# Kernel tuning notes

Hardware: AMD Instinct MI355X
Metric: run time of the kernel (lower is better)

Reference implementation:

```python
import jax, jax.numpy as jnp
import numpy as np

FOV_UP = 3.0 * np.pi / 180.0
FOV_DOWN = -25.0 * np.pi / 180.0
BIG = 1e9  # penalty to exclude invalid points from nearest-neighbor search


def rv_to_points(rv):
    """Spherical back-projection of a range image [H,W] -> xyz [H,W,3]."""
    H, W = rv.shape
    fov = FOV_UP - FOV_DOWN
    pitch = (1.0 - (jnp.arange(H, dtype=rv.dtype) + 0.5) / H) * fov + FOV_DOWN  # [H]
    yaw = -((jnp.arange(W, dtype=rv.dtype) + 0.5) / W * 2.0 - 1.0) * jnp.pi     # [W]
    cp = jnp.cos(pitch)[:, None]
    sp = jnp.sin(pitch)[:, None]
    x = rv * cp * jnp.cos(yaw)[None, :]
    y = rv * cp * jnp.sin(yaw)[None, :]
    z = rv * sp
    return jnp.stack([x, y, z], axis=-1)


def masked_chamfer(po, mo, pt, mt):
    """Symmetric chamfer (squared distances) between masked point sets.
    po [N,3], mo [N] in {0,1}; pt [M,3], mt [M] in {0,1}."""
    # squared pairwise distances [N,M] without materializing [N,M,3]
    d = (jnp.sum(po * po, axis=-1)[:, None]
         + jnp.sum(pt * pt, axis=-1)[None, :]
         - 2.0 * po @ pt.T)
    d1 = jnp.min(d + BIG * (1.0 - mt)[None, :], axis=1)  # NN dist for each output pt
    d2 = jnp.min(d + BIG * (1.0 - mo)[:, None], axis=0)  # NN dist for each target pt
    m1 = jnp.sum(d1 * mo) / jnp.maximum(jnp.sum(mo), 1.0)
    m2 = jnp.sum(d2 * mt) / jnp.maximum(jnp.sum(mt), 1.0)
    return m1 + m2


def chamfer_forward(rv, target):
    B, S, H, W = rv.shape

    def one(args):
        rv_bs, tgt_bs = args  # [H,W], [4,H,W]
        po = rv_to_points(rv_bs).reshape(-1, 3)
        mo = (rv_bs > 0.0).astype(rv_bs.dtype).reshape(-1)
        pt = jnp.transpose(tgt_bs[1:4], (1, 2, 0)).reshape(-1, 3)
        mt = (tgt_bs[0] > 0.0).astype(rv_bs.dtype).reshape(-1)
        return masked_chamfer(po, mo, pt, mt)

    # sequential over the B*S pairs: only one [N,N] distance matrix live at a time
    per_pair = jax.lax.map(one, (rv.reshape(B * S, H, W),
                                 target.reshape(B * S, 4, H, W)))
    return per_pair.reshape(B, S).T  # [S, B], matches chamfer_distances_tensor[s, b]


def setup_inputs():
    key = jax.random.key(0)
    k1, k2, k3 = jax.random.split(key, 3)
    B, S, H, W = 2, 4, 64, 128
    rv = jax.random.normal(k1, (B, S, H, W), dtype=jnp.float32)
    target = jax.random.normal(k2, (B, S, 4, H, W), dtype=jnp.float32)
    mos_label = jax.random.randint(k3, (B, S, H, W), 0, 2, dtype=jnp.int32)
    return {"rv": rv, "target": target, "mos_label": mos_label, "n_samples": -1}


def reference(rv, target, mos_label, n_samples):
    # n_samples == -1 -> full (non-subsampled) chamfer distance.
    # mos_label is extracted in the original but never affects the returned values.
    tensor = chamfer_forward(rv, target)          # [S, B]
    per_step = jnp.mean(tensor, axis=1)           # chamfer_distances[s] = batch mean
    return per_step, tensor
```

## Files before the change

kernel.cpp:

```cpp
#include <hip/hip_runtime.h>
#include <math.h>

constexpr int kH = 64, kW = 128, kB = 2, kS = 4;
constexpr int kNP = kH * kW;
constexpr int kPairs = kB * kS;
constexpr int kDirs = kPairs * 2;
constexpr float kPen = 32768.0f;
constexpr float kPi = 3.14159265358979323846f;
constexpr float kFovUp = 3.0f * kPi / 180.0f;
constexpr float kFovDown = -25.0f * kPi / 180.0f;

typedef short short8 __attribute__((ext_vector_type(8)));
typedef unsigned short ushort8 __attribute__((ext_vector_type(8)));
typedef float floatx4 __attribute__((ext_vector_type(4)));

constexpr int NCC = 8;
constexpr int CCH = kNP / NCC;
constexpr int NQB = 16;

constexpr size_t OFF_MIN = 524288;
constexpr size_t OFF_MVAL = 655360;
constexpr size_t OFF_DCNT = 655376;
constexpr size_t OFF_ACNT = 655392;

__device__ __forceinline__ unsigned short f2bf(float v) {
  unsigned u = __float_as_uint(v);
  unsigned r = u + 0x7FFFu + ((u >> 16) & 1u);
  return (unsigned short)(r >> 16);
}
__device__ __forceinline__ float bf2f(unsigned short b) {
  return __uint_as_float(((unsigned)b) << 16);
}


__global__ __launch_bounds__(256) void prep_kernel(
    const float* __restrict__ rv, const float* __restrict__ tgt,
    float4* __restrict__ pts, unsigned* __restrict__ minarr,
    float* __restrict__ mval, unsigned* __restrict__ dcnt,
    unsigned* __restrict__ acnt) {
  int idx = blockIdx.x * 256 + threadIdx.x;
  int p = idx >> 13;
  int k = idx & (kNP - 1);
  int h = k >> 7;
  int w = k & 127;

  float r = rv[idx];
  float pitch = (1.0f - (h + 0.5f) * (1.0f / kH)) * (kFovUp - kFovDown) + kFovDown;
  float yaw = -(((w + 0.5f) * (1.0f / kW)) * 2.0f - 1.0f) * kPi;
  float cp = __cosf(pitch), sp = __sinf(pitch);
  float cy = __cosf(yaw), sy = __sinf(yaw);
  float px = r * cp * cy, py = r * cp * sy, pz = r * sp;
  float mo = (r > 0.0f) ? 1.0f : 0.0f;

  const float* tb = tgt + (size_t)p * 4 * kNP;
  float mt = (tb[k] > 0.0f) ? 1.0f : 0.0f;
  float tx = tb[kNP + k], ty = tb[2 * kNP + k], tz = tb[3 * kNP + k];

  float no = px * px + py * py + pz * pz;
  float nt = tx * tx + ty * ty + tz * tz;
  float co = no + kPen * (1.0f - mo);
  float ct = nt + kPen * (1.0f - mt);

  int d0 = 2 * p, d1 = d0 + 1;
  pts[(size_t)d0 * kNP + k] = make_float4(px, py, pz, co);
  pts[(size_t)d1 * kNP + k] = make_float4(tx, ty, tz, ct);

  minarr[(size_t)d0 * kNP + k] = 0xFFFFFFFFu;
  minarr[(size_t)d1 * kNP + k] = 0xFFFFFFFFu;
  if (idx < kDirs) { dcnt[idx] = 0u; mval[idx] = 0.0f; }
  if (idx == kDirs) *acnt = 0u;
}

__global__ __launch_bounds__(256, 4) void nn_kernel(
    const float4* __restrict__ pts, unsigned* __restrict__ minarr,
    float* __restrict__ mval, unsigned* __restrict__ dcnt,
    unsigned* __restrict__ acnt, float* __restrict__ out) {
  __shared__ __align__(16) unsigned short sc[CCH * 16 + 16];
  __shared__ unsigned s_ticket;
  __shared__ float sw[4], sm[4];

  int bid = blockIdx.x;
  int d = bid >> 7;
  int qb = (bid >> 3) & 15;
  int ch = bid & 7;
  int t = threadIdx.x;

  const float4* cand = pts + (size_t)(d ^ 1) * kNP + ch * CCH;
#pragma unroll
  for (int i = 0; i < 4; ++i) {
    int j = t + i * 256;
    float4 P = cand[j];
    float X = -2.0f * P.x, Y = -2.0f * P.y, Z = -2.0f * P.z;
    float ct = P.w;
    unsigned short Xh = f2bf(X), Yh = f2bf(Y), Zh = f2bf(Z);
    unsigned short Xl = f2bf(X - bf2f(Xh));
    unsigned short Yl = f2bf(Y - bf2f(Yh));
    unsigned short Zl = f2bf(Z - bf2f(Zh));
    unsigned short Ch = f2bf(ct);
    float c1 = ct - bf2f(Ch);
    unsigned short Cl = f2bf(c1);
    unsigned short Cl2 = f2bf(c1 - bf2f(Cl));
    unsigned short* dst = sc + (j >> 4) * 256 + (j & 15) * 8;
    *(ushort8*)dst = (ushort8){Xh, Xl, Xh, Yh, Yl, Yh, Zh, Zl};
    *(ushort8*)(dst + 128) = (ushort8){Zh, Ch, Cl, Cl2, 0, 0, 0, 0};
  }
  if (t < 2) ((float4*)(sc + CCH * 16))[t] = make_float4(0.f, 0.f, 0.f, 0.f);
  __syncthreads();

  int wave = t >> 6, lane = t & 63;
  int n = lane & 15, q = lane >> 4;
  int qbase = d * kNP + qb * 512 + wave * 128;

  const short one_bf = (short)0x3F80;
  short8 bfr[8];
  float mn[8];
#pragma unroll
  for (int i = 0; i < 8; ++i) {
    short8 b = (short8){0, 0, 0, 0, 0, 0, 0, 0};
    if (q < 2) {
      float4 P = pts[qbase + i * 16 + n];
      unsigned short xh = f2bf(P.x), yh = f2bf(P.y), zh = f2bf(P.z);
      unsigned short xl = f2bf(P.x - bf2f(xh));
      unsigned short yl = f2bf(P.y - bf2f(yh));
      unsigned short zl = f2bf(P.z - bf2f(zh));
      if (q == 0)
        b = (short8){(short)xh, (short)xh, (short)xl, (short)yh,
                     (short)yh, (short)yl, (short)zh, (short)zh};
      else
        b = (short8){(short)zl, one_bf, one_bf, one_bf, 0, 0, 0, 0};
    }
    bfr[i] = b;
    mn[i] = 3.0e38f;
  }

  floatx4 zc = {0.0f, 0.0f, 0.0f, 0.0f};
  const unsigned short* aptr = (q < 2) ? (sc + q * 128 + n * 8) : (sc + CCH * 16);
  int astep = (q < 2) ? 256 : 0;

#pragma unroll 2
  for (int ctile = 0; ctile < CCH / 16; ++ctile) {
    short8 a = *(const short8*)aptr;
    aptr += astep;
#pragma unroll
    for (int i = 0; i < 8; ++i) {
      floatx4 dr = __builtin_amdgcn_mfma_f32_16x16x32_bf16(a, bfr[i], zc, 0, 0, 0);
      float u = fminf(fminf(dr[0], dr[1]), dr[2]);
      mn[i] = fminf(fminf(u, dr[3]), mn[i]);
    }
  }

#pragma unroll
  for (int i = 0; i < 8; ++i) {
    float m = mn[i];
    m = fminf(m, __shfl_xor(m, 16));
    m = fminf(m, __shfl_xor(m, 32));
    if (lane < 16) {
      unsigned bb = __float_as_uint(m);
      unsigned e = (bb & 0x80000000u) ? ~bb : (bb | 0x80000000u);
      atomicMin(&minarr[qbase + i * 16 + lane], e);
    }
  }

  __syncthreads();
  if (t == 0)
    s_ticket = __hip_atomic_fetch_add(&dcnt[d], 1u, __ATOMIC_RELAXED,
                                      __HIP_MEMORY_SCOPE_AGENT);
  __syncthreads();
  if (s_ticket != 127u) return;

  float wsum = 0.0f, msum = 0.0f;
#pragma unroll 4
  for (int j = 0; j < 32; ++j) {
    int k = j * 256 + t;
    unsigned u = __hip_atomic_load(&minarr[(size_t)d * kNP + k],
                                   __ATOMIC_RELAXED, __HIP_MEMORY_SCOPE_AGENT);
    unsigned bb = (u & 0x80000000u) ? (u ^ 0x80000000u) : ~u;
    float mnv = __uint_as_float(bb);
    float4 P = pts[(size_t)d * kNP + k];
    if (P.w < 16384.0f) {
      wsum += P.w + mnv;
      msum += 1.0f;
    }
  }
#pragma unroll
  for (int off = 32; off; off >>= 1) {
    wsum += __shfl_down(wsum, off);
    msum += __shfl_down(msum, off);
  }
  if ((t & 63) == 0) { sw[t >> 6] = wsum; sm[t >> 6] = msum; }
  __syncthreads();
  if (t == 0) {
    float ws_ = sw[0] + sw[1] + sw[2] + sw[3];
    float ms_ = sm[0] + sm[1] + sm[2] + sm[3];
    __hip_atomic_store(&mval[d], ws_ / fmaxf(ms_, 1.0f), __ATOMIC_RELAXED,
                       __HIP_MEMORY_SCOPE_AGENT);
    s_ticket = __hip_atomic_fetch_add(acnt, 1u, __ATOMIC_ACQ_REL,
                                      __HIP_MEMORY_SCOPE_AGENT);
  }
  __syncthreads();
  if (s_ticket != (unsigned)(kDirs - 1)) return;
  if (t == 0) {
    float mv[kDirs];
    for (int dd = 0; dd < kDirs; ++dd)
      mv[dd] = __hip_atomic_load(&mval[dd], __ATOMIC_RELAXED,
                                 __HIP_MEMORY_SCOPE_AGENT);
    for (int s = 0; s < kS; ++s) {
      float acc = 0.0f;
      for (int b = 0; b < kB; ++b) {
        int p = b * kS + s;
        float tens = mv[2 * p] + mv[2 * p + 1];
        out[kS + s * kB + b] = tens;
        acc += tens;
      }
      out[s] = acc * (1.0f / kB);
    }
  }
}

extern "C" void kernel_launch(void* const* d_in, const int* in_sizes, int n_in,
                              void* d_out, int out_size, void* d_ws, size_t ws_size,
                              hipStream_t stream) {
  const float* rv = (const float*)d_in[0];
  const float* tgt = (const float*)d_in[1];
  float* ws = (float*)d_ws;
  float4* pts = (float4*)ws;
  unsigned* minarr = (unsigned*)(ws + OFF_MIN);
  float* mval = ws + OFF_MVAL;
  unsigned* dcnt = (unsigned*)(ws + OFF_DCNT);
  unsigned* acnt = (unsigned*)(ws + OFF_ACNT);
  float* out = (float*)d_out;

  hipLaunchKernelGGL(prep_kernel, dim3(kPairs * kNP / 256), dim3(256), 0, stream,
                     rv, tgt, pts, minarr, mval, dcnt, acnt);
  hipLaunchKernelGGL(nn_kernel, dim3(kDirs * NQB * NCC), dim3(256), 0, stream,
                     pts, minarr, mval, dcnt, acnt, out);
}
```

Measured before the change: 116.6 us.

## Compute both chamfer directions from one distance tile with full-distance MFMA

The per-query norm is now folded into the MFMA operands, so each tile holds full squared distances. One pass per pair can then reduce both the row minima (output-to-target) and the column minima (target-to-output). Column minima are reduced with cross-lane shuffles into LDS atomics and then merged into global memory, which halves the grid and the total MFMA work. A constant bias keeps every distance positive so that raw float bit patterns can be used for atomicMin without the sign-flip encoding. The cost is extra shuffles and LDS atomics per tile in the inner loop.

```diff
diff --git a/kernel.cpp b/kernel.cpp
--- a/kernel.cpp
+++ b/kernel.cpp
@@ -6,6 +6,7 @@
 constexpr int kPairs = kB * kS;
 constexpr int kDirs = kPairs * 2;
 constexpr float kPen = 32768.0f;
+constexpr float kBias = 0.25f;
 constexpr float kPi = 3.14159265358979323846f;
 constexpr float kFovUp = 3.0f * kPi / 180.0f;
 constexpr float kFovDown = -25.0f * kPi / 180.0f;
@@ -17,6 +18,7 @@
 constexpr int NCC = 8;
 constexpr int CCH = kNP / NCC;
 constexpr int NQB = 16;
+constexpr int BPP = NQB * NCC;
 
 constexpr size_t OFF_MIN = 524288;
 constexpr size_t OFF_MVAL = 655360;
@@ -58,8 +60,8 @@
 
   float no = px * px + py * py + pz * pz;
   float nt = tx * tx + ty * ty + tz * tz;
-  float co = no + kPen * (1.0f - mo);
-  float ct = nt + kPen * (1.0f - mt);
+  float co = no + kPen * (1.0f - mo) + kBias;
+  float ct = nt + kPen * (1.0f - mt) + kBias;
 
   int d0 = 2 * p, d1 = d0 + 1;
   pts[(size_t)d0 * kNP + k] = make_float4(px, py, pz, co);
@@ -76,16 +78,19 @@
     float* __restrict__ mval, unsigned* __restrict__ dcnt,
     unsigned* __restrict__ acnt, float* __restrict__ out) {
   __shared__ __align__(16) unsigned short sc[CCH * 16 + 16];
+  __shared__ unsigned cminLds[CCH];
   __shared__ unsigned s_ticket;
-  __shared__ float sw[4], sm[4];
+  __shared__ float sred[16];
 
   int bid = blockIdx.x;
-  int d = bid >> 7;
+  int dp = bid >> 7;
+  int d0 = 2 * dp, d1 = d0 + 1;
   int qb = (bid >> 3) & 15;
   int ch = bid & 7;
   int t = threadIdx.x;
 
-  const float4* cand = pts + (size_t)(d ^ 1) * kNP + ch * CCH;
+  const float4* cand = pts + (size_t)d1 * kNP + ch * CCH;
+  const unsigned short one_bfu = 0x3F80;
 #pragma unroll
   for (int i = 0; i < 4; ++i) {
     int j = t + i * 256;
@@ -102,14 +107,17 @@
     unsigned short Cl2 = f2bf(c1 - bf2f(Cl));
     unsigned short* dst = sc + (j >> 4) * 256 + (j & 15) * 8;
     *(ushort8*)dst = (ushort8){Xh, Xl, Xh, Yh, Yl, Yh, Zh, Zl};
-    *(ushort8*)(dst + 128) = (ushort8){Zh, Ch, Cl, Cl2, 0, 0, 0, 0};
-  }
+    *(ushort8*)(dst + 128) =
+        (ushort8){Zh, Ch, Cl, Cl2, one_bfu, one_bfu, one_bfu, 0};
+  }
+#pragma unroll
+  for (int i = 0; i < 4; ++i) cminLds[t + i * 256] = 0xFFFFFFFFu;
   if (t < 2) ((float4*)(sc + CCH * 16))[t] = make_float4(0.f, 0.f, 0.f, 0.f);
   __syncthreads();
 
   int wave = t >> 6, lane = t & 63;
   int n = lane & 15, q = lane >> 4;
-  int qbase = d * kNP + qb * 512 + wave * 128;
+  int qbase = d0 * kNP + qb * 512 + wave * 128;
 
   const short one_bf = (short)0x3F80;
   short8 bfr[8];
@@ -123,11 +131,17 @@
       unsigned short xl = f2bf(P.x - bf2f(xh));
       unsigned short yl = f2bf(P.y - bf2f(yh));
       unsigned short zl = f2bf(P.z - bf2f(zh));
-      if (q == 0)
+      if (q == 0) {
         b = (short8){(short)xh, (short)xh, (short)xl, (short)yh,
                      (short)yh, (short)yl, (short)zh, (short)zh};
-      else
-        b = (short8){(short)zl, one_bf, one_bf, one_bf, 0, 0, 0, 0};
+      } else {
+        unsigned short Wh = f2bf(P.w);
+        float w1 = P.w - bf2f(Wh);
+        unsigned short Wl = f2bf(w1);
+        unsigned short Wl2 = f2bf(w1 - bf2f(Wl));
+        b = (short8){(short)zl, one_bf, one_bf, one_bf,
+                     (short)Wh, (short)Wl, (short)Wl2, 0};
+      }
     }
     bfr[i] = b;
     mn[i] = 3.0e38f;
@@ -136,16 +150,40 @@
   floatx4 zc = {0.0f, 0.0f, 0.0f, 0.0f};
   const unsigned short* aptr = (q < 2) ? (sc + q * 128 + n * 8) : (sc + CCH * 16);
   int astep = (q < 2) ? 256 : 0;
+  int cq4 = (lane >> 4) * 4;
+  bool leader = (n == 0);
 
 #pragma unroll 2
   for (int ctile = 0; ctile < CCH / 16; ++ctile) {
     short8 a = *(const short8*)aptr;
     aptr += astep;
-#pragma unroll
-    for (int i = 0; i < 8; ++i) {
-      floatx4 dr = __builtin_amdgcn_mfma_f32_16x16x32_bf16(a, bfr[i], zc, 0, 0, 0);
-      float u = fminf(fminf(dr[0], dr[1]), dr[2]);
-      mn[i] = fminf(fminf(u, dr[3]), mn[i]);
+    float c0 = 3.0e38f, c1 = 3.0e38f, c2 = 3.0e38f, c3 = 3.0e38f;
+#pragma unroll
+    for (int i = 0; i < 8; i += 2) {
+      floatx4 dA = __builtin_amdgcn_mfma_f32_16x16x32_bf16(a, bfr[i], zc, 0, 0, 0);
+      floatx4 dB = __builtin_amdgcn_mfma_f32_16x16x32_bf16(a, bfr[i + 1], zc, 0, 0, 0);
+      float uA = fminf(fminf(dA[0], dA[1]), dA[2]);
+      mn[i] = fminf(fminf(uA, dA[3]), mn[i]);
+      float uB = fminf(fminf(dB[0], dB[1]), dB[2]);
+      mn[i + 1] = fminf(fminf(uB, dB[3]), mn[i + 1]);
+      c0 = fminf(fminf(dA[0], dB[0]), c0);
+      c1 = fminf(fminf(dA[1], dB[1]), c1);
+      c2 = fminf(fminf(dA[2], dB[2]), c2);
+      c3 = fminf(fminf(dA[3], dB[3]), c3);
+    }
+#pragma unroll
+    for (int s = 1; s <= 8; s <<= 1) {
+      c0 = fminf(c0, __shfl_xor(c0, s));
+      c1 = fminf(c1, __shfl_xor(c1, s));
+      c2 = fminf(c2, __shfl_xor(c2, s));
+      c3 = fminf(c3, __shfl_xor(c3, s));
+    }
+    if (leader) {
+      unsigned* cp = cminLds + ctile * 16 + cq4;
+      atomicMin(cp + 0, __float_as_uint(c0));
+      atomicMin(cp + 1, __float_as_uint(c1));
+      atomicMin(cp + 2, __float_as_uint(c2));
+      atomicMin(cp + 3, __float_as_uint(c3));
     }
   }
 
@@ -154,51 +192,68 @@
     float m = mn[i];
     m = fminf(m, __shfl_xor(m, 16));
     m = fminf(m, __shfl_xor(m, 32));
-    if (lane < 16) {
-      unsigned bb = __float_as_uint(m);
-      unsigned e = (bb & 0x80000000u) ? ~bb : (bb | 0x80000000u);
-      atomicMin(&minarr[qbase + i * 16 + lane], e);
+    if (lane < 16)
+      atomicMin(&minarr[qbase + i * 16 + lane], __float_as_uint(m));
+  }
+
+  __syncthreads();
+  {
+    unsigned* garr = minarr + (size_t)d1 * kNP + ch * CCH;
+#pragma unroll
+    for (int i = 0; i < 4; ++i) {
+      int c = t + i * 256;
+      atomicMin(&garr[c], cminLds[c]);
     }
   }
 
   __syncthreads();
   if (t == 0)
-    s_ticket = __hip_atomic_fetch_add(&dcnt[d], 1u, __ATOMIC_RELAXED,
+    s_ticket = __hip_atomic_fetch_add(&dcnt[dp], 1u, __ATOMIC_RELAXED,
                                       __HIP_MEMORY_SCOPE_AGENT);
   __syncthreads();
-  if (s_ticket != 127u) return;
-
-  float wsum = 0.0f, msum = 0.0f;
-#pragma unroll 4
+  if (s_ticket != (unsigned)(BPP - 1)) return;
+
+  float ws0 = 0.0f, ms0 = 0.0f, ws1 = 0.0f, ms1 = 0.0f;
+#pragma unroll 2
   for (int j = 0; j < 32; ++j) {
     int k = j * 256 + t;
-    unsigned u = __hip_atomic_load(&minarr[(size_t)d * kNP + k],
-                                   __ATOMIC_RELAXED, __HIP_MEMORY_SCOPE_AGENT);
-    unsigned bb = (u & 0x80000000u) ? (u ^ 0x80000000u) : ~u;
-    float mnv = __uint_as_float(bb);
-    float4 P = pts[(size_t)d * kNP + k];
-    if (P.w < 16384.0f) {
-      wsum += P.w + mnv;
-      msum += 1.0f;
+    {
+      unsigned u = __hip_atomic_load(&minarr[(size_t)d0 * kNP + k],
+                                     __ATOMIC_RELAXED, __HIP_MEMORY_SCOPE_AGENT);
+      float4 P = pts[(size_t)d0 * kNP + k];
+      if (P.w < 16384.0f) { ws0 += __uint_as_float(u) - 2.0f * kBias; ms0 += 1.0f; }
+    }
+    {
+      unsigned u = __hip_atomic_load(&minarr[(size_t)d1 * kNP + k],
+                                     __ATOMIC_RELAXED, __HIP_MEMORY_SCOPE_AGENT);
+      float4 P = pts[(size_t)d1 * kNP + k];
+      if (P.w < 16384.0f) { ws1 += __uint_as_float(u) - 2.0f * kBias; ms1 += 1.0f; }
     }
   }
 #pragma unroll
   for (int off = 32; off; off >>= 1) {
-    wsum += __shfl_down(wsum, off);
-    msum += __shfl_down(msum, off);
-  }
-  if ((t & 63) == 0) { sw[t >> 6] = wsum; sm[t >> 6] = msum; }
+    ws0 += __shfl_down(ws0, off); ms0 += __shfl_down(ms0, off);
+    ws1 += __shfl_down(ws1, off); ms1 += __shfl_down(ms1, off);
+  }
+  if ((t & 63) == 0) {
+    int w = t >> 6;
+    sred[w] = ws0; sred[4 + w] = ms0; sred[8 + w] = ws1; sred[12 + w] = ms1;
+  }
   __syncthreads();
   if (t == 0) {
-    float ws_ = sw[0] + sw[1] + sw[2] + sw[3];
-    float ms_ = sm[0] + sm[1] + sm[2] + sm[3];
-    __hip_atomic_store(&mval[d], ws_ / fmaxf(ms_, 1.0f), __ATOMIC_RELAXED,
+    float W0 = sred[0] + sred[1] + sred[2] + sred[3];
+    float M0 = sred[4] + sred[5] + sred[6] + sred[7];
+    float W1 = sred[8] + sred[9] + sred[10] + sred[11];
+    float M1 = sred[12] + sred[13] + sred[14] + sred[15];
+    __hip_atomic_store(&mval[d0], W0 / fmaxf(M0, 1.0f), __ATOMIC_RELAXED,
+                       __HIP_MEMORY_SCOPE_AGENT);
+    __hip_atomic_store(&mval[d1], W1 / fmaxf(M1, 1.0f), __ATOMIC_RELAXED,
                        __HIP_MEMORY_SCOPE_AGENT);
     s_ticket = __hip_atomic_fetch_add(acnt, 1u, __ATOMIC_ACQ_REL,
                                       __HIP_MEMORY_SCOPE_AGENT);
   }
   __syncthreads();
-  if (s_ticket != (unsigned)(kDirs - 1)) return;
+  if (s_ticket != (unsigned)(kPairs - 1)) return;
   if (t == 0) {
     float mv[kDirs];
     for (int dd = 0; dd < kDirs; ++dd)
@@ -232,6 +287,6 @@
 
   hipLaunchKernelGGL(prep_kernel, dim3(kPairs * kNP / 256), dim3(256), 0, stream,
                      rv, tgt, pts, minarr, mval, dcnt, acnt);
-  hipLaunchKernelGGL(nn_kernel, dim3(kDirs * NQB * NCC), dim3(256), 0, stream,
+  hipLaunchKernelGGL(nn_kernel, dim3(kPairs * NQB * NCC), dim3(256), 0, stream,
                      pts, minarr, mval, dcnt, acnt, out);
 }
```

New measurement: 142.8 us. 1.22x slower.

## Switch distance tiles to 32x32x16 MFMA to remove wasted K lanes

Applied to the files above, without the earlier changes.

Replaces the 16x16x32 bf16 MFMA, whose upper K half was zero padding, with the 32x32x16 variant that packs the 13 split-precision terms into K=16. Query tiling and grid are reorganised to 1024 queries per block, with 32-wide query tiles per wave. The next candidate fragment is prefetched from LDS. This aims to cut wasted matrix-core work per distance, at the cost of more accumulator registers per MFMA and fewer blocks.

```diff
diff --git a/kernel.cpp b/kernel.cpp
--- a/kernel.cpp
+++ b/kernel.cpp
@@ -12,11 +12,13 @@
 
 typedef short short8 __attribute__((ext_vector_type(8)));
 typedef unsigned short ushort8 __attribute__((ext_vector_type(8)));
-typedef float floatx4 __attribute__((ext_vector_type(4)));
+typedef float floatx16 __attribute__((ext_vector_type(16)));
 
 constexpr int NCC = 8;
 constexpr int CCH = kNP / NCC;
-constexpr int NQB = 16;
+constexpr int NQB = 8;
+constexpr int BPD = NQB * NCC;
+constexpr int QT = 8;
 
 constexpr size_t OFF_MIN = 524288;
 constexpr size_t OFF_MVAL = 655360;
@@ -75,13 +77,13 @@
     const float4* __restrict__ pts, unsigned* __restrict__ minarr,
     float* __restrict__ mval, unsigned* __restrict__ dcnt,
     unsigned* __restrict__ acnt, float* __restrict__ out) {
-  __shared__ __align__(16) unsigned short sc[CCH * 16 + 16];
+  __shared__ __align__(16) unsigned short sc[CCH * 16 + 512];
   __shared__ unsigned s_ticket;
   __shared__ float sw[4], sm[4];
 
   int bid = blockIdx.x;
-  int d = bid >> 7;
-  int qb = (bid >> 3) & 15;
+  int d = bid >> 6;
+  int qb = (bid >> 3) & 7;
   int ch = bid & 7;
   int t = threadIdx.x;
 
@@ -100,64 +102,67 @@
     float c1 = ct - bf2f(Ch);
     unsigned short Cl = f2bf(c1);
     unsigned short Cl2 = f2bf(c1 - bf2f(Cl));
-    unsigned short* dst = sc + (j >> 4) * 256 + (j & 15) * 8;
+    unsigned short* dst = sc + (j >> 5) * 512 + (j & 31) * 8;
     *(ushort8*)dst = (ushort8){Xh, Xl, Xh, Yh, Yl, Yh, Zh, Zl};
-    *(ushort8*)(dst + 128) = (ushort8){Zh, Ch, Cl, Cl2, 0, 0, 0, 0};
-  }
-  if (t < 2) ((float4*)(sc + CCH * 16))[t] = make_float4(0.f, 0.f, 0.f, 0.f);
+    *(ushort8*)(dst + 256) = (ushort8){Zh, Ch, Cl, Cl2, 0, 0, 0, 0};
+  }
   __syncthreads();
 
   int wave = t >> 6, lane = t & 63;
-  int n = lane & 15, q = lane >> 4;
-  int qbase = d * kNP + qb * 512 + wave * 128;
+  int col = lane & 31, half = lane >> 5;
+  int qbase = d * kNP + qb * 1024 + wave * 256;
 
   const short one_bf = (short)0x3F80;
-  short8 bfr[8];
-  float mn[8];
-#pragma unroll
-  for (int i = 0; i < 8; ++i) {
-    short8 b = (short8){0, 0, 0, 0, 0, 0, 0, 0};
-    if (q < 2) {
-      float4 P = pts[qbase + i * 16 + n];
-      unsigned short xh = f2bf(P.x), yh = f2bf(P.y), zh = f2bf(P.z);
-      unsigned short xl = f2bf(P.x - bf2f(xh));
-      unsigned short yl = f2bf(P.y - bf2f(yh));
-      unsigned short zl = f2bf(P.z - bf2f(zh));
-      if (q == 0)
-        b = (short8){(short)xh, (short)xh, (short)xl, (short)yh,
-                     (short)yh, (short)yl, (short)zh, (short)zh};
-      else
-        b = (short8){(short)zl, one_bf, one_bf, one_bf, 0, 0, 0, 0};
-    }
-    bfr[i] = b;
-    mn[i] = 3.0e38f;
-  }
-
-  floatx4 zc = {0.0f, 0.0f, 0.0f, 0.0f};
-  const unsigned short* aptr = (q < 2) ? (sc + q * 128 + n * 8) : (sc + CCH * 16);
-  int astep = (q < 2) ? 256 : 0;
-
+  short8 bq[QT];
+  float mn[QT];
+#pragma unroll
+  for (int qt = 0; qt < QT; ++qt) {
+    float4 P = pts[qbase + qt * 32 + col];
+    unsigned short xh = f2bf(P.x), yh = f2bf(P.y), zh = f2bf(P.z);
+    unsigned short xl = f2bf(P.x - bf2f(xh));
+    unsigned short yl = f2bf(P.y - bf2f(yh));
+    unsigned short zl = f2bf(P.z - bf2f(zh));
+    short8 b;
+    if (half == 0)
+      b = (short8){(short)xh, (short)xh, (short)xl, (short)yh,
+                   (short)yh, (short)yl, (short)zh, (short)zh};
+    else
+      b = (short8){(short)zl, one_bf, one_bf, one_bf, 0, 0, 0, 0};
+    bq[qt] = b;
+    mn[qt] = 3.0e38f;
+  }
+
+  floatx16 zc = {0.0f, 0.0f, 0.0f, 0.0f, 0.0f, 0.0f, 0.0f, 0.0f,
+                 0.0f, 0.0f, 0.0f, 0.0f, 0.0f, 0.0f, 0.0f, 0.0f};
+
+  const short8* ap = (const short8*)sc + lane;
+  short8 a = ap[0];
 #pragma unroll 2
-  for (int ctile = 0; ctile < CCH / 16; ++ctile) {
-    short8 a = *(const short8*)aptr;
-    aptr += astep;
-#pragma unroll
-    for (int i = 0; i < 8; ++i) {
-      floatx4 dr = __builtin_amdgcn_mfma_f32_16x16x32_bf16(a, bfr[i], zc, 0, 0, 0);
-      float u = fminf(fminf(dr[0], dr[1]), dr[2]);
-      mn[i] = fminf(fminf(u, dr[3]), mn[i]);
-    }
-  }
-
-#pragma unroll
-  for (int i = 0; i < 8; ++i) {
-    float m = mn[i];
-    m = fminf(m, __shfl_xor(m, 16));
-    m = fminf(m, __shfl_xor(m, 32));
-    if (lane < 16) {
+  for (int ctile = 0; ctile < CCH / 32; ++ctile) {
+    short8 an = ap[(ctile + 1) * 64];
+#pragma unroll
+    for (int qt = 0; qt < QT; ++qt) {
+      floatx16 dr =
+          __builtin_amdgcn_mfma_f32_32x32x16_bf16(a, bq[qt], zc, 0, 0, 0);
+      float f0 = fminf(fminf(dr[0], dr[1]), dr[2]);
+      float f1 = fminf(fminf(dr[3], dr[4]), dr[5]);
+      float f2 = fminf(fminf(dr[6], dr[7]), dr[8]);
+      float f3 = fminf(fminf(dr[9], dr[10]), dr[11]);
+      float f4 = fminf(fminf(dr[12], dr[13]), dr[14]);
+      float g0 = fminf(fminf(f0, f1), dr[15]);
+      float g1 = fminf(fminf(f2, f3), f4);
+      mn[qt] = fminf(fminf(g0, g1), mn[qt]);
+    }
+    a = an;
+  }
+
+#pragma unroll
+  for (int qt = 0; qt < QT; ++qt) {
+    float m = fminf(mn[qt], __shfl_xor(mn[qt], 32));
+    if (lane < 32) {
       unsigned bb = __float_as_uint(m);
       unsigned e = (bb & 0x80000000u) ? ~bb : (bb | 0x80000000u);
-      atomicMin(&minarr[qbase + i * 16 + lane], e);
+      atomicMin(&minarr[qbase + qt * 32 + lane], e);
     }
   }
 
@@ -166,7 +171,7 @@
     s_ticket = __hip_atomic_fetch_add(&dcnt[d], 1u, __ATOMIC_RELAXED,
                                       __HIP_MEMORY_SCOPE_AGENT);
   __syncthreads();
-  if (s_ticket != 127u) return;
+  if (s_ticket != (unsigned)(BPD - 1)) return;
 
   float wsum = 0.0f, msum = 0.0f;
 #pragma unroll 4
```

Result: faster. 99.12 us (-15.0%).
